# Kernel tuning notes

Measured on AMD Instinct MI355X. Metric: run time of the kernel, lower is better.

## Reference

```python
import jax, jax.numpy as jnp
import numpy as np

B, L, HID, TRANS = 16384, 512, 768, 128


def setup_inputs() -> dict:
    key = jax.random.key(0)
    ks = jax.random.split(key, 12)
    def lin(k, out_d, in_d):
        kw, kb = jax.random.split(k)
        s = 1.0 / np.sqrt(in_d)
        return (jax.random.uniform(kw, (out_d, in_d), jnp.float32, -s, s),
                jax.random.uniform(kb, (out_d,), jnp.float32, -s, s))
    W_text, b_text = lin(ks[0], TRANS, HID)
    W_label, b_label = lin(ks[1], TRANS, HID)
    W0, b0 = lin(ks[2], TRANS, 2 * TRANS)
    W1, b1 = lin(ks[3], TRANS, TRANS)
    W2, b2 = lin(ks[4], 1, TRANS)
    target = jax.random.randint(ks[5], (B, L), 0, 2, jnp.int32)
    # guarantee every sample has at least one positive label (torch.mean on empty would NaN)
    target = target.at[:, 0].set(1)
    return {
        "text_embed": jax.random.normal(ks[6], (B, HID), jnp.float32),
        "label_embed": jax.random.normal(ks[7], (L, HID), jnp.float32),
        "target": target,
        "perm": jax.random.permutation(ks[8], B).astype(jnp.int32),
        "W_text": W_text, "b_text": b_text,
        "W_label": W_label, "b_label": b_label,
        "W0": W0, "b0": b0, "W1": W1, "b1": b1, "W2": W2, "b2": b2,
    }


def _network(t, l, W_text, b_text, W_label, b_label, W0, b0, W1, b1, W2, b2):
    tt = t @ W_text.T + b_text            # [B, trans]
    ll = l @ W_label.T + b_label          # [B, trans]
    h = jnp.concatenate([tt, ll], axis=1)  # [B, 2*trans]
    h = jax.nn.relu(h @ W0.T + b0)
    h = jax.nn.relu(h @ W1.T + b1)
    return h @ W2.T + b2                  # [B, 1]


def reference(text_embed, label_embed, target, perm,
              W_text, b_text, W_label, b_label, W0, b0, W1, b1, W2, b2):
    # variable-length mean pooling of label embeddings selected by the multi-hot target
    mask = target.astype(text_embed.dtype)                 # [B, L]
    counts = jnp.maximum(mask.sum(axis=1, keepdims=True), 1.0)
    label_feature_y = (mask @ label_embed) / counts        # [B, hid]
    negative_text = text_embed[perm]                       # shuffled negatives
    params = (W_text, b_text, W_label, b_label, W0, b0, W1, b1, W2, b2)
    E_joint = -jnp.mean(jax.nn.softplus(-_network(text_embed, label_feature_y, *params)))
    E_marginal = jnp.mean(jax.nn.softplus(_network(negative_text, label_feature_y, *params)))
    return E_marginal - E_joint
```

## Files before the change

### kernel.cpp

```cpp
#include <hip/hip_runtime.h>
#include <math.h>

#define BATCH 16384
#define LBL   512
#define HID   768
#define TR    128

typedef unsigned long long u64;
typedef unsigned short ushort_t;
typedef __attribute__((ext_vector_type(8))) short short8;
typedef __attribute__((ext_vector_type(4))) float f32x4;

__device__ __forceinline__ ushort_t f2bf(float f){
  unsigned u = __builtin_bit_cast(unsigned, f);
  u += 0x7FFFu + ((u >> 16) & 1u);
  return (ushort_t)(u >> 16);
}
__device__ __forceinline__ short8 pack8(float4 x, float4 y){
  short8 v;
  v[0]=(short)f2bf(x.x); v[1]=(short)f2bf(x.y); v[2]=(short)f2bf(x.z); v[3]=(short)f2bf(x.w);
  v[4]=(short)f2bf(y.x); v[5]=(short)f2bf(y.y); v[6]=(short)f2bf(y.z); v[7]=(short)f2bf(y.w);
  return v;
}
__device__ __forceinline__ float softplusf(float x){
  return fmaxf(x, 0.0f) + log1pf(expf(-fabsf(x)));
}
__device__ __forceinline__ void gload_lds16(const void* g, void* l){
  __builtin_amdgcn_global_load_lds((const __attribute__((address_space(1))) void*)g,
                                   (__attribute__((address_space(3))) void*)l, 16, 0, 0);
}

__global__ __launch_bounds__(256) void k1(
    const float* __restrict__ W0, const float* __restrict__ Wt, const float* __restrict__ Wl,
    const float* __restrict__ bt, const float* __restrict__ bl, const float* __restrict__ b0,
    const float* __restrict__ W1, const float* __restrict__ labe,
    ushort_t* __restrict__ Msw, ushort_t* __restrict__ W1B, ushort_t* __restrict__ Gt,
    float* __restrict__ KV, float* __restrict__ out){
  __shared__ __align__(16) char uni[50688];
  int bi = blockIdx.x, t = threadIdx.x;
  if (bi < 128){
    float* sw = (float*)uni;
    int i = bi;
    if (t < TR) sw[t] = W0[(size_t)i*256 + t];
    if (t < 128) W1B[i*128 + t] = f2bf(W1[i*128 + t]);
    __syncthreads();
    int c = t;
    float a0 = 0.f, a1 = 0.f, a2 = 0.f;
    #pragma unroll 8
    for (int a = 0; a < 128; a++){
      float w = sw[a];
      const float* r = Wt + (size_t)a*HID;
      a0 = fmaf(w, r[c], a0);
      a1 = fmaf(w, r[c+256], a1);
      a2 = fmaf(w, r[c+512], a2);
    }
    int c7 = c & 7;
    Msw[(((c      )>>3)<<10) + (i<<3) + c7] = f2bf(a0);
    Msw[(((c + 256)>>3)<<10) + (i<<3) + c7] = f2bf(a1);
    Msw[(((c + 512)>>3)<<10) + (i<<3) + c7] = f2bf(a2);
  } else if (bi == 128){
    if (t < TR){
      float s = b0[t];
      const float* r = W0 + (size_t)t*256;
      for (int a = 0; a < 128; a++) s = fmaf(r[a], bt[a], s);
      for (int a = 0; a < 128; a++) s = fmaf(r[128+a], bl[a], s);
      KV[t] = s;
    }
    if (t == 0) out[0] = 0.f;
  } else {
    int gi = bi - 129, l0 = gi * 32;
    int lane = t & 63, wave = t >> 6;
    int m = lane & 15, q = lane >> 4;
    ushort_t* Bs1 = (ushort_t*)uni;
    ushort_t* As1 = (ushort_t*)(uni + 32768);
    ushort_t* Pl  = (ushort_t*)(uni + 41984);

    int ar = t >> 3, ak = (t & 7) * 8;
    const float* apl = labe + (size_t)(l0 + ar)*HID + ak;
    int aB = t & 127, kh = t >> 7;
    const float* wlr = Wl + (size_t)aB*HID + kh*32;

    float4 ra0 = *(const float4*)apl;
    float4 ra1 = *(const float4*)(apl + 4);
    f32x4 accP[2][2];
    #pragma unroll
    for (int rt = 0; rt < 2; rt++)
      #pragma unroll
      for (int ct = 0; ct < 2; ct++) accP[rt][ct] = (f32x4){0.f,0.f,0.f,0.f};

    for (int c = 0; c < 12; c++){
      int buf = c & 1;
      #pragma unroll
      for (int j = 0; j < 4; j++){
        float4 w0v = *(const float4*)(wlr + c*64 + j*8);
        float4 w1v = *(const float4*)(wlr + c*64 + j*8 + 4);
        *(short8*)(Bs1 + buf*8192 + (kh*4 + j)*1024 + aB*8) = pack8(w0v, w1v);
      }
      *(short8*)(As1 + (size_t)(buf*32 + ar)*72 + ak) = pack8(ra0, ra1);
      __syncthreads();
      if (c < 11){
        ra0 = *(const float4*)(apl + (c+1)*64);
        ra1 = *(const float4*)(apl + (c+1)*64 + 4);
      }
      #pragma unroll
      for (int kcc = 0; kcc < 2; kcc++){
        short8 bfr[2];
        #pragma unroll
        for (int ct = 0; ct < 2; ct++)
          bfr[ct] = *(const short8*)(Bs1 + buf*8192 + (kcc*4 + q)*1024 + (wave*32 + ct*16 + m)*8);
        #pragma unroll
        for (int rt = 0; rt < 2; rt++){
          short8 a = *(const short8*)(As1 + (size_t)(buf*32 + rt*16 + m)*72 + kcc*32 + q*8);
          #pragma unroll
          for (int ct = 0; ct < 2; ct++)
            accP[rt][ct] = __builtin_amdgcn_mfma_f32_16x16x32_bf16(a, bfr[ct], accP[rt][ct], 0, 0, 0);
        }
      }
    }
    #pragma unroll
    for (int rt = 0; rt < 2; rt++)
      #pragma unroll
      for (int ct = 0; ct < 2; ct++){
        int col = wave*32 + ct*16 + m;
        #pragma unroll
        for (int r = 0; r < 4; r++)
          Pl[(size_t)(rt*16 + q*4 + r)*136 + col] = f2bf(accP[rt][ct][r]);
      }
    __syncthreads();

    int jB = t & 127, ah = t >> 7;
    const float* w0r = W0 + (size_t)jB*256 + 128 + ah*64;
    #pragma unroll
    for (int g2 = 0; g2 < 8; g2++){
      float4 u0 = *(const float4*)(w0r + g2*8);
      float4 u1 = *(const float4*)(w0r + g2*8 + 4);
      *(short8*)(Bs1 + (ah*8 + g2)*1024 + jB*8) = pack8(u0, u1);
    }
    __syncthreads();

    f32x4 accG[2][2];
    #pragma unroll
    for (int rt = 0; rt < 2; rt++)
      #pragma unroll
      for (int ct = 0; ct < 2; ct++) accG[rt][ct] = (f32x4){0.f,0.f,0.f,0.f};
    #pragma unroll
    for (int kc = 0; kc < 4; kc++){
      short8 bfr[2];
      #pragma unroll
      for (int ct = 0; ct < 2; ct++)
        bfr[ct] = *(const short8*)(Bs1 + (kc*4 + q)*1024 + (wave*32 + ct*16 + m)*8);
      #pragma unroll
      for (int rt = 0; rt < 2; rt++){
        short8 a = *(const short8*)(Pl + (size_t)(rt*16 + m)*136 + kc*32 + q*8);
        #pragma unroll
        for (int ct = 0; ct < 2; ct++)
          accG[rt][ct] = __builtin_amdgcn_mfma_f32_16x16x32_bf16(a, bfr[ct], accG[rt][ct], 0, 0, 0);
      }
    }
    #pragma unroll
    for (int rt = 0; rt < 2; rt++)
      #pragma unroll
      for (int ct = 0; ct < 2; ct++){
        int j = wave*32 + ct*16 + m;
        #pragma unroll
        for (int r = 0; r < 4; r++)
          Gt[(size_t)j*LBL + l0 + rt*16 + q*4 + r] = f2bf(accG[rt][ct][r]);
      }
  }
}

__global__ __launch_bounds__(512, 4) void k3(const float* __restrict__ T, const ushort_t* __restrict__ Msw,
                                          const float* __restrict__ KV, const ushort_t* __restrict__ Gt,
                                          const int* __restrict__ tgt,
                                          const int* __restrict__ perm, const ushort_t* __restrict__ W1b,
                                          const float* __restrict__ b1, const float* __restrict__ W2,
                                          const float* __restrict__ b2, float* __restrict__ out){
  __shared__ __align__(16) char uni[51200];
  __shared__ __align__(16) u64 bitsS[32*10];
  __shared__ float invs[32];

  int tid = threadIdx.x;
  int lane = tid & 63, wave = tid >> 6;
  int m = lane & 15, q = lane >> 4;
  int r0 = blockIdx.x * 32;
  ushort_t* Bs_ = (ushort_t*)uni;
  ushort_t* As_ = (ushort_t*)(uni + 32768);

  {
    const char* gb = (const char*)Msw;
    char* lb = (char*)Bs_;
    gload_lds16(gb + tid*16,        lb + tid*16);
    gload_lds16(gb + 8192 + tid*16, lb + 8192 + tid*16);
  }
  int vv[4][8];
  #pragma unroll
  for (int rr = 0; rr < 4; rr++){
    const int* rp = tgt + (size_t)(r0 + wave*4 + rr)*LBL;
    #pragma unroll
    for (int cc = 0; cc < 8; cc++) vv[rr][cc] = rp[cc*64 + lane];
  }
  int ar = tid >> 3, ak = (tid & 7) * 8;
  int arow = (ar < 32) ? (r0 + ar) : perm[r0 + ar - 32];
  const float* app = T + (size_t)arow*HID + ak;
  float4 aa0[2], aa1[2];
  aa0[0] = *(const float4*)(app);      aa1[0] = *(const float4*)(app + 4);
  aa0[1] = *(const float4*)(app + 64); aa1[1] = *(const float4*)(app + 68);

  #pragma unroll
  for (int rr = 0; rr < 4; rr++){
    int row = wave*4 + rr;
    int cnt = 0;
    #pragma unroll
    for (int cc = 0; cc < 8; cc++){
      u64 mm = __ballot(vv[rr][cc] != 0);
      if (lane == 0){ ((u64*)((char*)bitsS + row*80))[cc] = mm; cnt += __popcll(mm); }
    }
    if (lane == 0) invs[row] = 1.0f / (float)(cnt < 1 ? 1 : cnt);
  }

  f32x4 acc[4];
  #pragma unroll
  for (int rt = 0; rt < 4; rt++) acc[rt] = (f32x4){0.f,0.f,0.f,0.f};

  #pragma unroll
  for (int c = 0; c < 12; c++){
    int buf = c & 1;
    *(short8*)(As_ + (size_t)(buf*64 + ar)*72 + ak) = pack8(aa0[buf], aa1[buf]);
    if (c < 10){
      aa0[buf] = *(const float4*)(app + (c+2)*64);
      aa1[buf] = *(const float4*)(app + (c+2)*64 + 4);
    }
    __builtin_amdgcn_sched_barrier(0);
    if (c < 10) asm volatile("s_waitcnt vmcnt(2) lgkmcnt(0)" ::: "memory");
    else        asm volatile("s_waitcnt vmcnt(0) lgkmcnt(0)" ::: "memory");
    __builtin_amdgcn_s_barrier();
    __builtin_amdgcn_sched_barrier(0);
    if (c < 11){
      const char* gb = (const char*)Msw + (size_t)(c+1)*16384;
      char* lb = (char*)(Bs_ + (buf^1)*8192);
      gload_lds16(gb + tid*16,        lb + tid*16);
      gload_lds16(gb + 8192 + tid*16, lb + 8192 + tid*16);
    }
    __builtin_amdgcn_sched_barrier(0);
    __builtin_amdgcn_s_setprio(1);
    #pragma unroll
    for (int kcc = 0; kcc < 2; kcc++){
      short8 bfr = *(const short8*)(Bs_ + buf*8192 + (kcc*4 + q)*1024 + (wave*16 + m)*8);
      #pragma unroll
      for (int rt = 0; rt < 4; rt++){
        short8 a = *(const short8*)(As_ + (size_t)(buf*64 + rt*16 + m)*72 + kcc*32 + q*8);
        acc[rt] = __builtin_amdgcn_mfma_f32_16x16x32_bf16(a, bfr, acc[rt], 0, 0, 0);
      }
    }
    __builtin_amdgcn_s_setprio(0);
  }

  const unsigned char* bits_b = (const unsigned char*)bitsS;
  f32x4 accV[2] = {{0,0,0,0},{0,0,0,0}};
  const ushort_t* gp = Gt + (size_t)(wave*16 + m)*LBL + q*8;
  short8 bv0 = *(const short8*)(gp);
  short8 bv1 = *(const short8*)(gp + 32);
  for (int c = 0; c < 16; c++){
    short8 bn = bv1;
    if (c < 14) bn = *(const short8*)(gp + (size_t)(c+2)*32);
    #pragma unroll
    for (int rt = 0; rt < 2; rt++){
      unsigned bb = bits_b[(rt*16 + m)*80 + c*4 + q];
      short8 a;
      #pragma unroll
      for (int j = 0; j < 8; j++) a[j] = (short)(((bb >> j) & 1u) ? 0x3F80 : 0);
      accV[rt] = __builtin_amdgcn_mfma_f32_16x16x32_bf16(a, bv0, accV[rt], 0, 0, 0);
    }
    bv0 = bv1; bv1 = bn;
  }

  __syncthreads();
  ushort_t (*h0s)[136] = (ushort_t(*)[136])uni;
  float* sred = (float*)(uni + 17408);
  int col = wave*16 + m;
  float kv = KV[col];
  #pragma unroll
  for (int rt = 0; rt < 2; rt++){
    #pragma unroll
    for (int r = 0; r < 4; r++){
      int rowl = rt*16 + q*4 + r;
      float vvv = accV[rt][r] * invs[rowl] + kv;
      h0s[rowl][col]      = f2bf(fmaxf(acc[rt][r]   + vvv, 0.f));
      h0s[32 + rowl][col] = f2bf(fmaxf(acc[rt+2][r] + vvv, 0.f));
    }
  }
  __syncthreads();

  float w2c = W2[col], b1c = b1[col];
  float b2v = b2[0];
  #pragma unroll
  for (int rt2 = 0; rt2 < 4; rt2++){
    f32x4 accH = {0,0,0,0};
    #pragma unroll
    for (int kc = 0; kc < 4; kc++){
      short8 a = *(const short8*)&h0s[rt2*16 + m][kc*32 + q*8];
      short8 b = *(const short8*)(W1b + (size_t)col*TR + kc*32 + q*8);
      accH = __builtin_amdgcn_mfma_f32_16x16x32_bf16(a, b, accH, 0, 0, 0);
    }
    #pragma unroll
    for (int r = 0; r < 4; r++){
      float sp = w2c * fmaxf(accH[r] + b1c, 0.f);
      sred[(size_t)(rt2*16 + q*4 + r)*129 + col] = sp;
    }
  }
  __syncthreads();

  if (tid < 64){
    float s = b2v;
    #pragma unroll
    for (int n = 0; n < 128; n++) s += sred[(size_t)tid*129 + n];
    float val = (tid < 32) ? softplusf(-s) : softplusf(s);
    #pragma unroll
    for (int off = 32; off > 0; off >>= 1) val += __shfl_down(val, off);
    if (tid == 0) atomicAdd(out, val * (1.0f / (float)BATCH));
  }
}

extern "C" void kernel_launch(void* const* d_in, const int* in_sizes, int n_in,
                              void* d_out, int out_size, void* d_ws, size_t ws_size,
                              hipStream_t stream){
  const float* text = (const float*)d_in[0];
  const float* labe = (const float*)d_in[1];
  const int*   tgt  = (const int*)  d_in[2];
  const int*   perm = (const int*)  d_in[3];
  const float* Wt   = (const float*)d_in[4];
  const float* bt   = (const float*)d_in[5];
  const float* Wl   = (const float*)d_in[6];
  const float* bl   = (const float*)d_in[7];
  const float* W0   = (const float*)d_in[8];
  const float* b0   = (const float*)d_in[9];
  const float* W1   = (const float*)d_in[10];
  const float* b1   = (const float*)d_in[11];
  const float* W2   = (const float*)d_in[12];
  const float* b2   = (const float*)d_in[13];

  char* wsb = (char*)d_ws;
  size_t off = 0;
  auto alloc = [&](size_t bytes){
    size_t r = off;
    off += (bytes + 255) & ~(size_t)255;
    return r;
  };
  ushort_t* MSW = (ushort_t*)(wsb + alloc((size_t)TR*HID*2));
  ushort_t* GT  = (ushort_t*)(wsb + alloc((size_t)TR*LBL*2));
  ushort_t* W1B = (ushort_t*)(wsb + alloc((size_t)TR*TR*2));
  float*    KV  = (float*)   (wsb + alloc((size_t)TR*4));
  float*    out = (float*)d_out;
  (void)ws_size; (void)in_sizes; (void)n_in; (void)out_size;

  k1<<<145, 256, 0, stream>>>(W0, Wt, Wl, bt, bl, b0, W1, labe, MSW, W1B, GT, KV, out);
  k3<<<512, 512, 0, stream>>>(text, MSW, KV, GT, tgt, perm, W1B, b1, W2, b2, out);
}
```

Before: 168.9 us.

## Split fused kernel: compute text projection once per row, gather via perm later

```diff
diff --git a/kernel.cpp b/kernel.cpp
--- a/kernel.cpp
+++ b/kernel.cpp
@@ -25,16 +25,12 @@
 __device__ __forceinline__ float softplusf(float x){
   return fmaxf(x, 0.0f) + log1pf(expf(-fabsf(x)));
 }
-__device__ __forceinline__ void gload_lds16(const void* g, void* l){
-  __builtin_amdgcn_global_load_lds((const __attribute__((address_space(1))) void*)g,
-                                   (__attribute__((address_space(3))) void*)l, 16, 0, 0);
-}
 
 __global__ __launch_bounds__(256) void k1(
     const float* __restrict__ W0, const float* __restrict__ Wt, const float* __restrict__ Wl,
     const float* __restrict__ bt, const float* __restrict__ bl, const float* __restrict__ b0,
     const float* __restrict__ W1, const float* __restrict__ labe,
-    ushort_t* __restrict__ Msw, ushort_t* __restrict__ W1B, ushort_t* __restrict__ Gt,
+    ushort_t* __restrict__ Mp, ushort_t* __restrict__ W1B, ushort_t* __restrict__ Gt,
     float* __restrict__ KV, float* __restrict__ out){
   __shared__ __align__(16) char uni[50688];
   int bi = blockIdx.x, t = threadIdx.x;
@@ -54,10 +50,9 @@
       a1 = fmaf(w, r[c+256], a1);
       a2 = fmaf(w, r[c+512], a2);
     }
-    int c7 = c & 7;
-    Msw[(((c      )>>3)<<10) + (i<<3) + c7] = f2bf(a0);
-    Msw[(((c + 256)>>3)<<10) + (i<<3) + c7] = f2bf(a1);
-    Msw[(((c + 512)>>3)<<10) + (i<<3) + c7] = f2bf(a2);
+    Mp[(size_t)i*HID + c]       = f2bf(a0);
+    Mp[(size_t)i*HID + c + 256] = f2bf(a1);
+    Mp[(size_t)i*HID + c + 512] = f2bf(a2);
   } else if (bi == 128){
     if (t < TR){
       float s = b0[t];
@@ -169,156 +164,200 @@
   }
 }
 
-__global__ __launch_bounds__(512, 4) void k3(const float* __restrict__ T, const ushort_t* __restrict__ Msw,
-                                          const float* __restrict__ KV, const ushort_t* __restrict__ Gt,
-                                          const int* __restrict__ tgt,
-                                          const int* __restrict__ perm, const ushort_t* __restrict__ W1b,
-                                          const float* __restrict__ b1, const float* __restrict__ W2,
-                                          const float* __restrict__ b2, float* __restrict__ out){
-  __shared__ __align__(16) char uni[51200];
-  __shared__ __align__(16) u64 bitsS[32*10];
-  __shared__ float invs[32];
-
+__global__ __launch_bounds__(512, 4) void kU(
+    const float* __restrict__ T, const int* __restrict__ tgt,
+    const ushort_t* __restrict__ Mp, const ushort_t* __restrict__ Gt,
+    const float* __restrict__ KVg,
+    float* __restrict__ U, float* __restrict__ W){
+  __shared__ __align__(16) ushort_t sB[32*768];
+  int bid = blockIdx.x;
+  int xcd = bid & 7, slot = bid >> 3;
+  int rg = xcd*16 + (slot >> 2), cg = slot & 3;
+  int r0 = rg * 128, c0 = cg * 32;
   int tid = threadIdx.x;
-  int lane = tid & 63, wave = tid >> 6;
+  int lane = tid & 63, w = tid >> 6;
   int m = lane & 15, q = lane >> 4;
-  int r0 = blockIdx.x * 32;
-  ushort_t* Bs_ = (ushort_t*)uni;
-  ushort_t* As_ = (ushort_t*)(uni + 32768);
 
   {
-    const char* gb = (const char*)Msw;
-    char* lb = (char*)Bs_;
-    gload_lds16(gb + tid*16,        lb + tid*16);
-    gload_lds16(gb + 8192 + tid*16, lb + 8192 + tid*16);
-  }
-  int vv[4][8];
-  #pragma unroll
-  for (int rr = 0; rr < 4; rr++){
-    const int* rp = tgt + (size_t)(r0 + wave*4 + rr)*LBL;
-    #pragma unroll
-    for (int cc = 0; cc < 8; cc++) vv[rr][cc] = rp[cc*64 + lane];
-  }
-  int ar = tid >> 3, ak = (tid & 7) * 8;
-  int arow = (ar < 32) ? (r0 + ar) : perm[r0 + ar - 32];
-  const float* app = T + (size_t)arow*HID + ak;
-  float4 aa0[2], aa1[2];
-  aa0[0] = *(const float4*)(app);      aa1[0] = *(const float4*)(app + 4);
-  aa0[1] = *(const float4*)(app + 64); aa1[1] = *(const float4*)(app + 68);
-
-  #pragma unroll
-  for (int rr = 0; rr < 4; rr++){
-    int row = wave*4 + rr;
-    int cnt = 0;
-    #pragma unroll
-    for (int cc = 0; cc < 8; cc++){
-      u64 mm = __ballot(vv[rr][cc] != 0);
-      if (lane == 0){ ((u64*)((char*)bitsS + row*80))[cc] = mm; cnt += __popcll(mm); }
-    }
-    if (lane == 0) invs[row] = 1.0f / (float)(cnt < 1 ? 1 : cnt);
-  }
-
-  f32x4 acc[4];
-  #pragma unroll
-  for (int rt = 0; rt < 4; rt++) acc[rt] = (f32x4){0.f,0.f,0.f,0.f};
-
-  #pragma unroll
-  for (int c = 0; c < 12; c++){
-    int buf = c & 1;
-    *(short8*)(As_ + (size_t)(buf*64 + ar)*72 + ak) = pack8(aa0[buf], aa1[buf]);
-    if (c < 10){
-      aa0[buf] = *(const float4*)(app + (c+2)*64);
-      aa1[buf] = *(const float4*)(app + (c+2)*64 + 4);
-    }
-    __builtin_amdgcn_sched_barrier(0);
-    if (c < 10) asm volatile("s_waitcnt vmcnt(2) lgkmcnt(0)" ::: "memory");
-    else        asm volatile("s_waitcnt vmcnt(0) lgkmcnt(0)" ::: "memory");
-    __builtin_amdgcn_s_barrier();
-    __builtin_amdgcn_sched_barrier(0);
-    if (c < 11){
-      const char* gb = (const char*)Msw + (size_t)(c+1)*16384;
-      char* lb = (char*)(Bs_ + (buf^1)*8192);
-      gload_lds16(gb + tid*16,        lb + tid*16);
-      gload_lds16(gb + 8192 + tid*16, lb + 8192 + tid*16);
-    }
-    __builtin_amdgcn_sched_barrier(0);
-    __builtin_amdgcn_s_setprio(1);
-    #pragma unroll
-    for (int kcc = 0; kcc < 2; kcc++){
-      short8 bfr = *(const short8*)(Bs_ + buf*8192 + (kcc*4 + q)*1024 + (wave*16 + m)*8);
-      #pragma unroll
-      for (int rt = 0; rt < 4; rt++){
-        short8 a = *(const short8*)(As_ + (size_t)(buf*64 + rt*16 + m)*72 + kcc*32 + q*8);
-        acc[rt] = __builtin_amdgcn_mfma_f32_16x16x32_bf16(a, bfr, acc[rt], 0, 0, 0);
-      }
-    }
-    __builtin_amdgcn_s_setprio(0);
-  }
-
-  const unsigned char* bits_b = (const unsigned char*)bitsS;
+    int n = tid >> 4, o = (tid & 15) * 16;
+    const char* src = (const char*)Mp + (size_t)(c0 + n)*1536 + o;
+    char* dst = (char*)sB + n*1536;
+    int sx = (n & 7) << 4;
+    #pragma unroll
+    for (int j = 0; j < 6; j++){
+      int off = o + j*256;
+      *(short8*)(dst + (off ^ sx)) = *(const short8*)(src + j*256);
+    }
+  }
+  __syncthreads();
+
+  int row = r0 + w*16 + m;
+  const float* tp = T + (size_t)row*HID + q*8;
+  float4 pf0[3], pf1[3];
+  #pragma unroll
+  for (int d = 0; d < 3; d++){
+    pf0[d] = *(const float4*)(tp + d*32);
+    pf1[d] = *(const float4*)(tp + d*32 + 4);
+  }
+
+  f32x4 acc[2] = {{0,0,0,0},{0,0,0,0}};
+  #pragma unroll
+  for (int kc = 0; kc < 24; kc++){
+    int s = kc % 3;
+    short8 af = pack8(pf0[s], pf1[s]);
+    if (kc < 21){
+      pf0[s] = *(const float4*)(tp + (kc+3)*32);
+      pf1[s] = *(const float4*)(tp + (kc+3)*32 + 4);
+    }
+    #pragma unroll
+    for (int ct = 0; ct < 2; ct++){
+      int n = ct*16 + m;
+      short8 bf = *(const short8*)((const char*)sB + n*1536 + ((kc*64 + q*16) ^ ((n&7)<<4)));
+      acc[ct] = __builtin_amdgcn_mfma_f32_16x16x32_bf16(af, bf, acc[ct], 0, 0, 0);
+    }
+  }
+  __syncthreads();
+
+  {
+    int n = tid >> 4, o = (tid & 15) * 16;
+    const char* src = (const char*)Gt + (size_t)(c0 + n)*1024 + o;
+    char* dst = (char*)sB + n*1024;
+    int sx = (n & 7) << 4;
+    #pragma unroll
+    for (int j = 0; j < 4; j++){
+      int off = o + j*256;
+      *(short8*)(dst + (off ^ sx)) = *(const short8*)(src + j*256);
+    }
+  }
+  __syncthreads();
+
+  const int* gtp = tgt + (size_t)row*LBL + q*8;
+  int4 tf0[2], tf1[2];
+  #pragma unroll
+  for (int d = 0; d < 2; d++){
+    tf0[d] = *(const int4*)(gtp + d*32);
+    tf1[d] = *(const int4*)(gtp + d*32 + 4);
+  }
   f32x4 accV[2] = {{0,0,0,0},{0,0,0,0}};
-  const ushort_t* gp = Gt + (size_t)(wave*16 + m)*LBL + q*8;
-  short8 bv0 = *(const short8*)(gp);
-  short8 bv1 = *(const short8*)(gp + 32);
-  for (int c = 0; c < 16; c++){
-    short8 bn = bv1;
-    if (c < 14) bn = *(const short8*)(gp + (size_t)(c+2)*32);
-    #pragma unroll
-    for (int rt = 0; rt < 2; rt++){
-      unsigned bb = bits_b[(rt*16 + m)*80 + c*4 + q];
-      short8 a;
-      #pragma unroll
-      for (int j = 0; j < 8; j++) a[j] = (short)(((bb >> j) & 1u) ? 0x3F80 : 0);
-      accV[rt] = __builtin_amdgcn_mfma_f32_16x16x32_bf16(a, bv0, accV[rt], 0, 0, 0);
-    }
-    bv0 = bv1; bv1 = bn;
-  }
-
+  int cnt = 0;
+  #pragma unroll
+  for (int lc = 0; lc < 16; lc++){
+    int s = lc & 1;
+    int4 x0 = tf0[s], x1 = tf1[s];
+    if (lc < 14){
+      tf0[s] = *(const int4*)(gtp + (lc+2)*32);
+      tf1[s] = *(const int4*)(gtp + (lc+2)*32 + 4);
+    }
+    short8 af;
+    af[0] = x0.x ? (short)0x3F80 : (short)0;
+    af[1] = x0.y ? (short)0x3F80 : (short)0;
+    af[2] = x0.z ? (short)0x3F80 : (short)0;
+    af[3] = x0.w ? (short)0x3F80 : (short)0;
+    af[4] = x1.x ? (short)0x3F80 : (short)0;
+    af[5] = x1.y ? (short)0x3F80 : (short)0;
+    af[6] = x1.z ? (short)0x3F80 : (short)0;
+    af[7] = x1.w ? (short)0x3F80 : (short)0;
+    cnt += (x0.x!=0) + (x0.y!=0) + (x0.z!=0) + (x0.w!=0)
+         + (x1.x!=0) + (x1.y!=0) + (x1.z!=0) + (x1.w!=0);
+    #pragma unroll
+    for (int ct = 0; ct < 2; ct++){
+      int n = ct*16 + m;
+      short8 bf = *(const short8*)((const char*)sB + n*1024 + ((lc*64 + q*16) ^ ((n&7)<<4)));
+      accV[ct] = __builtin_amdgcn_mfma_f32_16x16x32_bf16(af, bf, accV[ct], 0, 0, 0);
+    }
+  }
+  cnt += __shfl_xor(cnt, 16);
+  cnt += __shfl_xor(cnt, 32);
+  float invm = 1.0f / (float)(cnt < 1 ? 1 : cnt);
+
+  float kvc[2];
+  kvc[0] = KVg[c0 + m];
+  kvc[1] = KVg[c0 + 16 + m];
+  #pragma unroll
+  for (int ct = 0; ct < 2; ct++){
+    #pragma unroll
+    for (int r = 0; r < 4; r++){
+      int rr = q*4 + r;
+      float invr = __shfl(invm, rr);
+      size_t o = (size_t)(r0 + w*16 + rr)*TR + c0 + ct*16 + m;
+      U[o] = acc[ct][r];
+      W[o] = accV[ct][r]*invr + kvc[ct];
+    }
+  }
+}
+
+__global__ __launch_bounds__(256, 4) void kT(
+    const float* __restrict__ U, const float* __restrict__ W,
+    const int* __restrict__ perm, const ushort_t* __restrict__ W1b,
+    const float* __restrict__ b1, const float* __restrict__ W2,
+    const float* __restrict__ b2, float* __restrict__ out){
+  __shared__ float sp4[4];
+  int tid = threadIdx.x;
+  int lane = tid & 63, w = tid >> 6;
+  int m = lane & 15, q = lane >> 4;
+  int gw = blockIdx.x*4 + w;
+  int half = gw & 1;
+  int rbase = (gw >> 1) * 16;
+  int row = rbase + m;
+  int srow = half ? perm[row] : row;
+  const float* up = U + (size_t)srow*TR + q*8;
+  const float* wp = W + (size_t)row*TR + q*8;
+
+  f32x4 acc[8];
+  #pragma unroll
+  for (int ct = 0; ct < 8; ct++) acc[ct] = (f32x4){0.f,0.f,0.f,0.f};
+
+  #pragma unroll
+  for (int kc = 0; kc < 4; kc++){
+    float4 u0 = *(const float4*)(up + kc*32);
+    float4 u1 = *(const float4*)(up + kc*32 + 4);
+    float4 w0 = *(const float4*)(wp + kc*32);
+    float4 w1 = *(const float4*)(wp + kc*32 + 4);
+    short8 af;
+    af[0] = (short)f2bf(fmaxf(u0.x + w0.x, 0.f));
+    af[1] = (short)f2bf(fmaxf(u0.y + w0.y, 0.f));
+    af[2] = (short)f2bf(fmaxf(u0.z + w0.z, 0.f));
+    af[3] = (short)f2bf(fmaxf(u0.w + w0.w, 0.f));
+    af[4] = (short)f2bf(fmaxf(u1.x + w1.x, 0.f));
+    af[5] = (short)f2bf(fmaxf(u1.y + w1.y, 0.f));
+    af[6] = (short)f2bf(fmaxf(u1.z + w1.z, 0.f));
+    af[7] = (short)f2bf(fmaxf(u1.w + w1.w, 0.f));
+    #pragma unroll
+    for (int ct = 0; ct < 8; ct++){
+      short8 bf = *(const short8*)(W1b + (size_t)(ct*16 + m)*TR + kc*32 + q*8);
+      acc[ct] = __builtin_amdgcn_mfma_f32_16x16x32_bf16(af, bf, acc[ct], 0, 0, 0);
+    }
+  }
+
+  float b2v = b2[0];
+  float sr[4] = {0.f, 0.f, 0.f, 0.f};
+  #pragma unroll
+  for (int ct = 0; ct < 8; ct++){
+    int col = ct*16 + m;
+    float w2c = W2[col], b1c = b1[col];
+    #pragma unroll
+    for (int r = 0; r < 4; r++)
+      sr[r] = fmaf(w2c, fmaxf(acc[ct][r] + b1c, 0.f), sr[r]);
+  }
+  #pragma unroll
+  for (int r = 0; r < 4; r++){
+    sr[r] += __shfl_xor(sr[r], 1);
+    sr[r] += __shfl_xor(sr[r], 2);
+    sr[r] += __shfl_xor(sr[r], 4);
+    sr[r] += __shfl_xor(sr[r], 8);
+  }
+  float val = 0.f;
+  #pragma unroll
+  for (int r = 0; r < 4; r++){
+    float s = sr[r] + b2v;
+    val += half ? softplusf(s) : softplusf(-s);
+  }
+  val += __shfl_xor(val, 16);
+  val += __shfl_xor(val, 32);
+  if (lane == 0) sp4[w] = val;
   __syncthreads();
-  ushort_t (*h0s)[136] = (ushort_t(*)[136])uni;
-  float* sred = (float*)(uni + 17408);
-  int col = wave*16 + m;
-  float kv = KV[col];
-  #pragma unroll
-  for (int rt = 0; rt < 2; rt++){
-    #pragma unroll
-    for (int r = 0; r < 4; r++){
-      int rowl = rt*16 + q*4 + r;
-      float vvv = accV[rt][r] * invs[rowl] + kv;
-      h0s[rowl][col]      = f2bf(fmaxf(acc[rt][r]   + vvv, 0.f));
-      h0s[32 + rowl][col] = f2bf(fmaxf(acc[rt+2][r] + vvv, 0.f));
-    }
-  }
-  __syncthreads();
-
-  float w2c = W2[col], b1c = b1[col];
-  float b2v = b2[0];
-  #pragma unroll
-  for (int rt2 = 0; rt2 < 4; rt2++){
-    f32x4 accH = {0,0,0,0};
-    #pragma unroll
-    for (int kc = 0; kc < 4; kc++){
-      short8 a = *(const short8*)&h0s[rt2*16 + m][kc*32 + q*8];
-      short8 b = *(const short8*)(W1b + (size_t)col*TR + kc*32 + q*8);
-      accH = __builtin_amdgcn_mfma_f32_16x16x32_bf16(a, b, accH, 0, 0, 0);
-    }
-    #pragma unroll
-    for (int r = 0; r < 4; r++){
-      float sp = w2c * fmaxf(accH[r] + b1c, 0.f);
-      sred[(size_t)(rt2*16 + q*4 + r)*129 + col] = sp;
-    }
-  }
-  __syncthreads();
-
-  if (tid < 64){
-    float s = b2v;
-    #pragma unroll
-    for (int n = 0; n < 128; n++) s += sred[(size_t)tid*129 + n];
-    float val = (tid < 32) ? softplusf(-s) : softplusf(s);
-    #pragma unroll
-    for (int off = 32; off > 0; off >>= 1) val += __shfl_down(val, off);
-    if (tid == 0) atomicAdd(out, val * (1.0f / (float)BATCH));
-  }
+  if (tid == 0)
+    atomicAdd(out, (sp4[0] + sp4[1] + sp4[2] + sp4[3]) * (1.0f / (float)BATCH));
 }
 
 extern "C" void kernel_launch(void* const* d_in, const int* in_sizes, int n_in,
@@ -346,13 +385,16 @@
     off += (bytes + 255) & ~(size_t)255;
     return r;
   };
-  ushort_t* MSW = (ushort_t*)(wsb + alloc((size_t)TR*HID*2));
+  ushort_t* MP  = (ushort_t*)(wsb + alloc((size_t)TR*HID*2));
   ushort_t* GT  = (ushort_t*)(wsb + alloc((size_t)TR*LBL*2));
   ushort_t* W1B = (ushort_t*)(wsb + alloc((size_t)TR*TR*2));
   float*    KV  = (float*)   (wsb + alloc((size_t)TR*4));
+  float*    UW_ = (float*)   (wsb + alloc((size_t)BATCH*TR*4));
+  float*    WW_ = (float*)   (wsb + alloc((size_t)BATCH*TR*4));
   float*    out = (float*)d_out;
   (void)ws_size; (void)in_sizes; (void)n_in; (void)out_size;
 
-  k1<<<145, 256, 0, stream>>>(W0, Wt, Wl, bt, bl, b0, W1, labe, MSW, W1B, GT, KV, out);
-  k3<<<512, 512, 0, stream>>>(text, MSW, KV, GT, tgt, perm, W1B, b1, W2, b2, out);
-}
+  k1<<<145, 256, 0, stream>>>(W0, Wt, Wl, bt, bl, b0, W1, labe, MP, W1B, GT, KV, out);
+  kU<<<512, 512, 0, stream>>>(text, tgt, MP, GT, KV, UW_, WW_);
+  kT<<<512, 256, 0, stream>>>(UW_, WW_, perm, W1B, b1, W2, b2, out);
+}
```

Measured after the change: 200.5 us. 18.7% more time.

## Interleave label-mask MFMA pass into the text GEMM main loop

Applied to the files above, without the earlier changes.

```diff
diff --git a/kernel.cpp b/kernel.cpp
--- a/kernel.cpp
+++ b/kernel.cpp
@@ -218,7 +218,10 @@
     if (lane == 0) invs[row] = 1.0f / (float)(cnt < 1 ? 1 : cnt);
   }
 
+  const ushort_t* gp = Gt + (size_t)(wave*16 + m)*LBL + q*8;
+  short8 gbuf[2][2];
   f32x4 acc[4];
+  f32x4 accV[2] = {{0,0,0,0},{0,0,0,0}};
   #pragma unroll
   for (int rt = 0; rt < 4; rt++) acc[rt] = (f32x4){0.f,0.f,0.f,0.f};
 
@@ -230,9 +233,16 @@
       aa0[buf] = *(const float4*)(app + (c+2)*64);
       aa1[buf] = *(const float4*)(app + (c+2)*64 + 4);
     }
+    if (c >= 3 && c < 11){
+      int sbase = 2*(c-3);
+      gbuf[(c+1)&1][0] = *(const short8*)(gp + (size_t)sbase*32);
+      gbuf[(c+1)&1][1] = *(const short8*)(gp + (size_t)(sbase+1)*32);
+    }
     __builtin_amdgcn_sched_barrier(0);
-    if (c < 10) asm volatile("s_waitcnt vmcnt(2) lgkmcnt(0)" ::: "memory");
-    else        asm volatile("s_waitcnt vmcnt(0) lgkmcnt(0)" ::: "memory");
+    if (c < 3)        asm volatile("s_waitcnt vmcnt(2) lgkmcnt(0)" ::: "memory");
+    else if (c < 10)  asm volatile("s_waitcnt vmcnt(4) lgkmcnt(0)" ::: "memory");
+    else if (c == 10) asm volatile("s_waitcnt vmcnt(2) lgkmcnt(0)" ::: "memory");
+    else              asm volatile("s_waitcnt vmcnt(0) lgkmcnt(0)" ::: "memory");
     __builtin_amdgcn_s_barrier();
     __builtin_amdgcn_sched_barrier(0);
     if (c < 11){
@@ -252,26 +262,26 @@
         acc[rt] = __builtin_amdgcn_mfma_f32_16x16x32_bf16(a, bfr, acc[rt], 0, 0, 0);
       }
     }
+    if (c >= 4){
+      u64 w0 = *(const u64*)((const char*)bitsS + (size_t)m*80      + (size_t)(c-4)*8);
+      u64 w1 = *(const u64*)((const char*)bitsS + (size_t)(16+m)*80 + (size_t)(c-4)*8);
+      u64 s0 = w0 >> (q*8);
+      u64 s1 = w1 >> (q*8);
+      #pragma unroll
+      for (int sl = 0; sl < 2; sl++){
+        unsigned b0 = (unsigned)(s0 >> (sl*32)) & 0xffu;
+        unsigned b1 = (unsigned)(s1 >> (sl*32)) & 0xffu;
+        short8 a0f, a1f;
+        #pragma unroll
+        for (int j = 0; j < 8; j++){
+          a0f[j] = (short)(((b0 >> j) & 1u) ? 0x3F80 : 0);
+          a1f[j] = (short)(((b1 >> j) & 1u) ? 0x3F80 : 0);
+        }
+        accV[0] = __builtin_amdgcn_mfma_f32_16x16x32_bf16(a0f, gbuf[c&1][sl], accV[0], 0, 0, 0);
+        accV[1] = __builtin_amdgcn_mfma_f32_16x16x32_bf16(a1f, gbuf[c&1][sl], accV[1], 0, 0, 0);
+      }
+    }
     __builtin_amdgcn_s_setprio(0);
-  }
-
-  const unsigned char* bits_b = (const unsigned char*)bitsS;
-  f32x4 accV[2] = {{0,0,0,0},{0,0,0,0}};
-  const ushort_t* gp = Gt + (size_t)(wave*16 + m)*LBL + q*8;
-  short8 bv0 = *(const short8*)(gp);
-  short8 bv1 = *(const short8*)(gp + 32);
-  for (int c = 0; c < 16; c++){
-    short8 bn = bv1;
-    if (c < 14) bn = *(const short8*)(gp + (size_t)(c+2)*32);
-    #pragma unroll
-    for (int rt = 0; rt < 2; rt++){
-      unsigned bb = bits_b[(rt*16 + m)*80 + c*4 + q];
-      short8 a;
-      #pragma unroll
-      for (int j = 0; j < 8; j++) a[j] = (short)(((bb >> j) & 1u) ? 0x3F80 : 0);
-      accV[rt] = __builtin_amdgcn_mfma_f32_16x16x32_bf16(a, bv0, accV[rt], 0, 0, 0);
-    }
-    bv0 = bv1; bv1 = bn;
   }
 
   __syncthreads();
```

Result: slower. 173.1 us (+2.5%).

## Load A operands directly into registers and interleave label-mean GEMM into main loop

Applied to the files above, without the earlier changes.

```diff
diff --git a/kernel.cpp b/kernel.cpp
--- a/kernel.cpp
+++ b/kernel.cpp
@@ -21,6 +21,14 @@
   v[0]=(short)f2bf(x.x); v[1]=(short)f2bf(x.y); v[2]=(short)f2bf(x.z); v[3]=(short)f2bf(x.w);
   v[4]=(short)f2bf(y.x); v[5]=(short)f2bf(y.y); v[6]=(short)f2bf(y.z); v[7]=(short)f2bf(y.w);
   return v;
+}
+__device__ __forceinline__ short8 pack8_cvt(float4 x, float4 y){
+  union { short8 s; unsigned u[4]; } r;
+  asm("v_cvt_pk_bf16_f32 %0, %1, %2" : "=v"(r.u[0]) : "v"(x.x), "v"(x.y));
+  asm("v_cvt_pk_bf16_f32 %0, %1, %2" : "=v"(r.u[1]) : "v"(x.z), "v"(x.w));
+  asm("v_cvt_pk_bf16_f32 %0, %1, %2" : "=v"(r.u[2]) : "v"(y.x), "v"(y.y));
+  asm("v_cvt_pk_bf16_f32 %0, %1, %2" : "=v"(r.u[3]) : "v"(y.z), "v"(y.w));
+  return r.s;
 }
 __device__ __forceinline__ float softplusf(float x){
   return fmaxf(x, 0.0f) + log1pf(expf(-fabsf(x)));
@@ -170,21 +178,21 @@
 }
 
 __global__ __launch_bounds__(512, 4) void k3(const float* __restrict__ T, const ushort_t* __restrict__ Msw,
-                                          const float* __restrict__ KV, const ushort_t* __restrict__ Gt,
+                                          const float* __restrict__ KVg, const ushort_t* __restrict__ Gt,
                                           const int* __restrict__ tgt,
                                           const int* __restrict__ perm, const ushort_t* __restrict__ W1b,
                                           const float* __restrict__ b1, const float* __restrict__ W2,
                                           const float* __restrict__ b2, float* __restrict__ out){
-  __shared__ __align__(16) char uni[51200];
+  __shared__ __align__(16) char uni[67328];
   __shared__ __align__(16) u64 bitsS[32*10];
   __shared__ float invs[32];
 
   int tid = threadIdx.x;
-  int lane = tid & 63, wave = tid >> 6;
+  int lane = tid & 63, w = tid >> 6;
   int m = lane & 15, q = lane >> 4;
+  int rt4 = w >> 1, ch = w & 1;
   int r0 = blockIdx.x * 32;
   ushort_t* Bs_ = (ushort_t*)uni;
-  ushort_t* As_ = (ushort_t*)(uni + 32768);
 
   {
     const char* gb = (const char*)Msw;
@@ -195,20 +203,22 @@
   int vv[4][8];
   #pragma unroll
   for (int rr = 0; rr < 4; rr++){
-    const int* rp = tgt + (size_t)(r0 + wave*4 + rr)*LBL;
+    const int* rp = tgt + (size_t)(r0 + w*4 + rr)*LBL;
     #pragma unroll
     for (int cc = 0; cc < 8; cc++) vv[rr][cc] = rp[cc*64 + lane];
   }
-  int ar = tid >> 3, ak = (tid & 7) * 8;
-  int arow = (ar < 32) ? (r0 + ar) : perm[r0 + ar - 32];
-  const float* app = T + (size_t)arow*HID + ak;
-  float4 aa0[2], aa1[2];
-  aa0[0] = *(const float4*)(app);      aa1[0] = *(const float4*)(app + 4);
-  aa0[1] = *(const float4*)(app + 64); aa1[1] = *(const float4*)(app + 68);
+  int gr = (rt4 < 2) ? (r0 + rt4*16 + m) : perm[r0 + (rt4 - 2)*16 + m];
+  const float* ap = T + (size_t)gr*HID + q*8;
+  float4 fa[2][2][2];
+  #pragma unroll
+  for (int kcc = 0; kcc < 2; kcc++){
+    fa[0][kcc][0] = *(const float4*)(ap + kcc*32);
+    fa[0][kcc][1] = *(const float4*)(ap + kcc*32 + 4);
+  }
 
   #pragma unroll
   for (int rr = 0; rr < 4; rr++){
-    int row = wave*4 + rr;
+    int row = w*4 + rr;
     int cnt = 0;
     #pragma unroll
     for (int cc = 0; cc < 8; cc++){
@@ -218,24 +228,43 @@
     if (lane == 0) invs[row] = 1.0f / (float)(cnt < 1 ? 1 : cnt);
   }
 
+  const ushort_t* gpt[2];
+  #pragma unroll
+  for (int ct = 0; ct < 2; ct++)
+    gpt[ct] = Gt + (size_t)((w>>1)*32 + ct*16 + m)*LBL + q*8;
+  int vrow = (w & 1)*16 + m;
+
+  short8 gbuf[2][2][2];
   f32x4 acc[4];
-  #pragma unroll
-  for (int rt = 0; rt < 4; rt++) acc[rt] = (f32x4){0.f,0.f,0.f,0.f};
+  f32x4 accV[2] = {{0,0,0,0},{0,0,0,0}};
+  #pragma unroll
+  for (int ct = 0; ct < 4; ct++) acc[ct] = (f32x4){0.f,0.f,0.f,0.f};
 
   #pragma unroll
   for (int c = 0; c < 12; c++){
     int buf = c & 1;
-    *(short8*)(As_ + (size_t)(buf*64 + ar)*72 + ak) = pack8(aa0[buf], aa1[buf]);
-    if (c < 10){
-      aa0[buf] = *(const float4*)(app + (c+2)*64);
-      aa1[buf] = *(const float4*)(app + (c+2)*64 + 4);
+    if (c <= 10){
+      #pragma unroll
+      for (int kcc = 0; kcc < 2; kcc++){
+        fa[(c+1)&1][kcc][0] = *(const float4*)(ap + (c+1)*64 + kcc*32);
+        fa[(c+1)&1][kcc][1] = *(const float4*)(ap + (c+1)*64 + kcc*32 + 4);
+      }
+    }
+    if (c >= 3 && c <= 10){
+      int sb = 2*(c-3);
+      #pragma unroll
+      for (int sl = 0; sl < 2; sl++)
+        #pragma unroll
+        for (int ct = 0; ct < 2; ct++)
+          gbuf[(c+1)&1][sl][ct] = *(const short8*)(gpt[ct] + (size_t)(sb + sl)*32);
     }
     __builtin_amdgcn_sched_barrier(0);
-    if (c < 10) asm volatile("s_waitcnt vmcnt(2) lgkmcnt(0)" ::: "memory");
-    else        asm volatile("s_waitcnt vmcnt(0) lgkmcnt(0)" ::: "memory");
+    if (c == 11)    asm volatile("s_waitcnt vmcnt(0) lgkmcnt(0)" ::: "memory");
+    else if (c < 3) asm volatile("s_waitcnt vmcnt(4) lgkmcnt(0)" ::: "memory");
+    else            asm volatile("s_waitcnt vmcnt(8) lgkmcnt(0)" ::: "memory");
     __builtin_amdgcn_s_barrier();
     __builtin_amdgcn_sched_barrier(0);
-    if (c < 11){
+    if (c <= 10){
       const char* gb = (const char*)Msw + (size_t)(c+1)*16384;
       char* lb = (char*)(Bs_ + (buf^1)*8192);
       gload_lds16(gb + tid*16,        lb + tid*16);
@@ -245,53 +274,60 @@
     __builtin_amdgcn_s_setprio(1);
     #pragma unroll
     for (int kcc = 0; kcc < 2; kcc++){
-      short8 bfr = *(const short8*)(Bs_ + buf*8192 + (kcc*4 + q)*1024 + (wave*16 + m)*8);
-      #pragma unroll
-      for (int rt = 0; rt < 4; rt++){
-        short8 a = *(const short8*)(As_ + (size_t)(buf*64 + rt*16 + m)*72 + kcc*32 + q*8);
-        acc[rt] = __builtin_amdgcn_mfma_f32_16x16x32_bf16(a, bfr, acc[rt], 0, 0, 0);
+      short8 a = pack8_cvt(fa[c&1][kcc][0], fa[c&1][kcc][1]);
+      #pragma unroll
+      for (int ct = 0; ct < 4; ct++){
+        short8 bfr = *(const short8*)(Bs_ + buf*8192 + (kcc*4 + q)*1024 + (ch*64 + ct*16 + m)*8);
+        acc[ct] = __builtin_amdgcn_mfma_f32_16x16x32_bf16(a, bfr, acc[ct], 0, 0, 0);
+      }
+    }
+    if (c >= 4){
+      u64 w0 = *(const u64*)((const char*)bitsS + (size_t)vrow*80 + (size_t)(c-4)*8);
+      u64 s0 = w0 >> (q*8);
+      #pragma unroll
+      for (int sl = 0; sl < 2; sl++){
+        unsigned bb = (unsigned)(s0 >> (sl*32)) & 0xffu;
+        short8 af;
+        #pragma unroll
+        for (int j = 0; j < 8; j++) af[j] = (short)(((bb >> j) & 1u) ? 0x3F80 : 0);
+        #pragma unroll
+        for (int ct = 0; ct < 2; ct++)
+          accV[ct] = __builtin_amdgcn_mfma_f32_16x16x32_bf16(af, gbuf[c&1][sl][ct], accV[ct], 0, 0, 0);
       }
     }
     __builtin_amdgcn_s_setprio(0);
   }
 
-  const unsigned char* bits_b = (const unsigned char*)bitsS;
-  f32x4 accV[2] = {{0,0,0,0},{0,0,0,0}};
-  const ushort_t* gp = Gt + (size_t)(wave*16 + m)*LBL + q*8;
-  short8 bv0 = *(const short8*)(gp);
-  short8 bv1 = *(const short8*)(gp + 32);
-  for (int c = 0; c < 16; c++){
-    short8 bn = bv1;
-    if (c < 14) bn = *(const short8*)(gp + (size_t)(c+2)*32);
-    #pragma unroll
-    for (int rt = 0; rt < 2; rt++){
-      unsigned bb = bits_b[(rt*16 + m)*80 + c*4 + q];
-      short8 a;
-      #pragma unroll
-      for (int j = 0; j < 8; j++) a[j] = (short)(((bb >> j) & 1u) ? 0x3F80 : 0);
-      accV[rt] = __builtin_amdgcn_mfma_f32_16x16x32_bf16(a, bv0, accV[rt], 0, 0, 0);
-    }
-    bv0 = bv1; bv1 = bn;
-  }
-
   __syncthreads();
-  ushort_t (*h0s)[136] = (ushort_t(*)[136])uni;
-  float* sred = (float*)(uni + 17408);
-  int col = wave*16 + m;
-  float kv = KV[col];
-  #pragma unroll
-  for (int rt = 0; rt < 2; rt++){
+  float* sV = (float*)uni;
+  #pragma unroll
+  for (int ct = 0; ct < 2; ct++){
+    int vc = (w>>1)*32 + ct*16 + m;
+    float kv = KVg[vc];
     #pragma unroll
     for (int r = 0; r < 4; r++){
-      int rowl = rt*16 + q*4 + r;
-      float vvv = accV[rt][r] * invs[rowl] + kv;
-      h0s[rowl][col]      = f2bf(fmaxf(acc[rt][r]   + vvv, 0.f));
-      h0s[32 + rowl][col] = f2bf(fmaxf(acc[rt+2][r] + vvv, 0.f));
+      int vr = (w & 1)*16 + q*4 + r;
+      sV[(size_t)vr*132 + vc] = accV[ct][r]*invs[vr] + kv;
     }
   }
   __syncthreads();
 
-  float w2c = W2[col], b1c = b1[col];
+  ushort_t (*h0s)[136] = (ushort_t(*)[136])(uni + 16896);
+  #pragma unroll
+  for (int ct = 0; ct < 4; ct++){
+    int col = ch*64 + ct*16 + m;
+    #pragma unroll
+    for (int r = 0; r < 4; r++){
+      int urow = rt4*16 + q*4 + r;
+      float vw = sV[(size_t)(urow & 31)*132 + col];
+      h0s[urow][col] = f2bf(fmaxf(acc[ct][r] + vw, 0.f));
+    }
+  }
+  __syncthreads();
+
+  float* sred = (float*)(uni + 34304);
+  int colh = w*16 + m;
+  float w2c = W2[colh], b1c = b1[colh];
   float b2v = b2[0];
   #pragma unroll
   for (int rt2 = 0; rt2 < 4; rt2++){
@@ -299,13 +335,13 @@
     #pragma unroll
     for (int kc = 0; kc < 4; kc++){
       short8 a = *(const short8*)&h0s[rt2*16 + m][kc*32 + q*8];
-      short8 b = *(const short8*)(W1b + (size_t)col*TR + kc*32 + q*8);
+      short8 b = *(const short8*)(W1b + (size_t)colh*TR + kc*32 + q*8);
       accH = __builtin_amdgcn_mfma_f32_16x16x32_bf16(a, b, accH, 0, 0, 0);
     }
     #pragma unroll
     for (int r = 0; r < 4; r++){
       float sp = w2c * fmaxf(accH[r] + b1c, 0.f);
-      sred[(size_t)(rt2*16 + q*4 + r)*129 + col] = sp;
+      sred[(size_t)(rt2*16 + q*4 + r)*129 + colh] = sp;
     }
   }
   __syncthreads();
```

Measured after the change: 189.0 us. 1.12x slower.
